# Kernel optimization log

Measured on AMD Instinct MI355X. Metric: run time of the kernel, lower is better.

The kernel has to match this reference:

```python
import jax, jax.numpy as jnp
import numpy as np

NUM_CODES = 4096
EMBED_DIM = 64
BETA = 0.25


def setup_inputs() -> dict:
    key = jax.random.key(0)
    k1, k2 = jax.random.split(key)
    z = jax.random.normal(k1, (8, EMBED_DIM, 64, 64), dtype=jnp.float32)
    weight = jax.random.normal(k2, (NUM_CODES, EMBED_DIM), dtype=jnp.float32)
    return {"z": z, "weight": weight}


def reference(z, weight):
    # z: [B, C, H, W] -> [B, H, W, C]
    z_bhwc = jnp.moveaxis(z, 1, -1)
    z_flat = z_bhwc.reshape(-1, EMBED_DIM)  # [N, d]

    # squared-euclidean distances: ||z||^2 + ||w||^2 - 2 z.w  -> [N, num_codes]
    distance = (
        jnp.sum(z_flat ** 2, axis=1, keepdims=True)
        + jnp.sum(weight ** 2, axis=1)
        - 2.0 * jnp.einsum('bd,nd->bn', z_flat, weight)
    )
    encoding_indices = jnp.argmin(distance, axis=1)  # [N]

    # codebook lookup (gather)
    z_q = weight[encoding_indices].reshape(z_bhwc.shape)  # [B, H, W, C]

    encodings = jax.nn.one_hot(encoding_indices, NUM_CODES, dtype=z.dtype)  # [N, num_codes]
    avg_probs = jnp.mean(encodings, axis=0)
    tiny = 1e-10  # max(1e-10, finfo(fp32).tiny)
    perplexity = jnp.exp(-jnp.sum(avg_probs * jnp.log(avg_probs + tiny)))

    # commitment loss (z_q detached) — eval path, no EMA state update
    loss = BETA * jnp.mean((jax.lax.stop_gradient(z_q) - z_bhwc) ** 2)

    # straight-through estimator
    z_q = z_bhwc + jax.lax.stop_gradient(z_q - z_bhwc)
    z_q = jnp.moveaxis(z_q, -1, 1)  # back to [B, C, H, W]

    return z_q, loss, perplexity, encodings, encoding_indices
```

## Files before the change

### kernel.cpp

```cpp
#include <hip/hip_runtime.h>
#include <math.h>
#include <float.h>

#define ZQ_OFF   0
#define LOSS_OFF 2097152
#define PERP_OFF 2097153
#define ENC_OFF  2097154
#define IDX_OFF  136314882ULL
#define BETA     0.25f


typedef __attribute__((ext_vector_type(8))) short short8;
typedef __attribute__((ext_vector_type(4))) float f32x4;

#define MFMA16(a, b, c) __builtin_amdgcn_mfma_f32_16x16x32_bf16(a, b, c, 0, 0, 0)

__device__ __forceinline__ float bf16_rn(float v, unsigned short* h) {
    unsigned u = __float_as_uint(v);
    unsigned r = (u + 0x7fffu + ((u >> 16) & 1u)) & 0xffff0000u;
    *h = (unsigned short)(r >> 16);
    return __uint_as_float(r);
}
__device__ __forceinline__ void split3(float v, unsigned short* h, unsigned short* m, unsigned short* l) {
    float hf = bf16_rn(v, h);
    float r1 = v - hf;
    float mf = bf16_rn(r1, m);
    float r2 = r1 - mf;
    bf16_rn(r2, l);
}

__global__ void vq_wnorm(const float* __restrict__ w, float* __restrict__ wnorm) {
    int c = blockIdx.x * 256 + threadIdx.x;
    const float4* w4 = (const float4*)(w + ((size_t)c << 6));
    float s = 0.f;
    #pragma unroll
    for (int k = 0; k < 16; ++k) { float4 v = w4[k]; s += v.x*v.x + v.y*v.y + v.z*v.z + v.w*v.w; }
    wnorm[c] = s;
}

__global__ void vq_prep(const float* __restrict__ w, unsigned short* __restrict__ w3) {
    int u = blockIdx.x * 256 + threadIdx.x;
    int c = u >> 5, slot = u & 31;
    if (slot >= 24) return;
    int p = slot >> 3, g = slot & 7;
    float4 v0 = *(const float4*)(w + ((size_t)c << 6) + g * 8);
    float4 v1 = *(const float4*)(w + ((size_t)c << 6) + g * 8 + 4);
    float vv[8] = {v0.x, v0.y, v0.z, v0.w, v1.x, v1.y, v1.z, v1.w};
    short8 o;
    #pragma unroll
    for (int e = 0; e < 8; ++e) {
        unsigned short h, m, l;
        split3(vv[e], &h, &m, &l);
        o[e] = (short)((p == 0) ? h : (p == 1) ? m : l);
    }
    char* dst = (char*)w3 + (size_t)c * 384 + (((unsigned)slot * 16) ^ (((unsigned)c & 7) << 4));
    *(short8*)dst = o;
}

__global__ __launch_bounds__(256, 2) void vq_main(
    const float* __restrict__ z, const float* __restrict__ w,
    const float* __restrict__ wnorm, const unsigned short* __restrict__ w3,
    float* __restrict__ out,
    float* __restrict__ loss_ws, int* __restrict__ ticket, int* __restrict__ hist)
{
    __shared__ __align__(16) char wl[2 * 24576];
    __shared__ float snorm[4096];
    __shared__ int s_widx[64];
    __shared__ int s_flag;

    const int tx   = threadIdx.x;
    const int lane = tx & 63;
    const int wv   = tx >> 6;
    const int lcol = lane & 15;
    const int lkq  = lane >> 4;
    const int base = blockIdx.x * 64;
    const int bb   = base >> 12;
    const int hh   = (base & 4095) >> 6;

    const char* w3b = (const char*)w3;

    {
        const char* s0 = w3b + wv * 6144 + (size_t)lane * 16;
        char* d0 = wl + wv * 6144;
        #pragma unroll
        for (int i = 0; i < 6; ++i)
            __builtin_amdgcn_global_load_lds(
                (const __attribute__((address_space(1))) void*)(s0 + i * 1024),
                (__attribute__((address_space(3))) void*)(d0 + i * 1024), 16, 0, 0);
    }

    float (*zS)[64] = (float (*)[64])(wl + 24576);
    #pragma unroll
    for (int j = 0; j < 4; ++j) {
        int f4 = j * 256 + tx;
        int d  = f4 >> 4, w4i = f4 & 15;
        float4 v = *(const float4*)(z + (((size_t)bb * 64 + d) * 64 + hh) * 64 + w4i * 4);
        *(float4*)&zS[d][w4i * 4] = v;
    }
    #pragma unroll
    for (int j = 0; j < 4; ++j) {
        int c4 = (j * 256 + tx) * 4;
        *(float4*)&snorm[c4] = *(const float4*)(wnorm + c4);
    }
    __syncthreads();

    short8 aH[2], aM[2], aL[2];
    #pragma unroll
    for (int s = 0; s < 2; ++s)
        #pragma unroll
        for (int j = 0; j < 8; ++j) {
            float v = zS[s * 32 + lkq * 8 + j][wv * 16 + lcol];
            unsigned short h, m, l;
            split3(v, &h, &m, &l);
            aH[s][j] = (short)h; aM[s][j] = (short)m; aL[s][j] = (short)l;
        }
    __builtin_amdgcn_sched_barrier(0);
    __builtin_amdgcn_s_barrier();
    __builtin_amdgcn_sched_barrier(0);

    float best[4]; int bidx[4];
    #pragma unroll
    for (int r = 0; r < 4; ++r) { best[r] = FLT_MAX; bidx[r] = 0; }

    float* enc = out + ENC_OFF;
    const unsigned sw = ((unsigned)lcol & 7) << 4;

    #pragma unroll 1
    for (int ch = 0; ch < 64; ++ch) {
        const char* cur = wl + (ch & 1) * 24576;
        char*       nxt = wl + (~ch & 1) * 24576;

        {
            const char* s0 = w3b + (size_t)((ch + 1) & 63) * 24576 + wv * 6144 + (size_t)lane * 16;
            char* d0 = nxt + wv * 6144;
            #pragma unroll
            for (int i = 0; i < 6; ++i)
                __builtin_amdgcn_global_load_lds(
                    (const __attribute__((address_space(1))) void*)(s0 + i * 1024),
                    (__attribute__((address_space(3))) void*)(d0 + i * 1024), 16, 0, 0);
        }
        {
            float2* rowp = (float2*)(enc + ((size_t)(base + ch) << 12));
            #pragma unroll
            for (int j = 0; j < 8; ++j)
                rowp[wv * 512 + j * 64 + lane] = make_float2(0.f, 0.f);
        }
        __builtin_amdgcn_sched_barrier(0);
        asm volatile("s_waitcnt vmcnt(14)" ::: "memory");
        __builtin_amdgcn_s_barrier();
        __builtin_amdgcn_sched_barrier(0);

        {
            const int cbase = ch << 6;
            float wnv[4];
            #pragma unroll
            for (int t = 0; t < 4; ++t) wnv[t] = snorm[cbase + t * 16 + lcol];
            #pragma unroll 2
            for (int t = 0; t < 4; ++t) {
                const int clocal = t * 16 + lcol;
                const char* rowp = cur + clocal * 384;
                short8 bH0 = *(const short8*)(rowp + ((lkq * 16      ) ^ sw));
                short8 bH1 = *(const short8*)(rowp + ((lkq * 16 +  64) ^ sw));
                short8 bM0 = *(const short8*)(rowp + ((lkq * 16 + 128) ^ sw));
                short8 bM1 = *(const short8*)(rowp + ((lkq * 16 + 192) ^ sw));
                short8 bL0 = *(const short8*)(rowp + ((lkq * 16 + 256) ^ sw));
                short8 bL1 = *(const short8*)(rowp + ((lkq * 16 + 320) ^ sw));
                f32x4 c0 = {0.f, 0.f, 0.f, 0.f}, c1 = {0.f, 0.f, 0.f, 0.f}, c2 = {0.f, 0.f, 0.f, 0.f};
                c0 = MFMA16(aH[0], bH0, c0); c0 = MFMA16(aH[1], bH1, c0);
                c1 = MFMA16(aH[0], bM0, c1); c1 = MFMA16(aH[1], bM1, c1);
                c1 = MFMA16(aM[0], bH0, c1); c1 = MFMA16(aM[1], bH1, c1);
                c2 = MFMA16(aM[0], bM0, c2); c2 = MFMA16(aM[1], bM1, c2);
                c2 = MFMA16(aH[0], bL0, c2); c2 = MFMA16(aH[1], bL1, c2);
                c2 = MFMA16(aL[0], bH0, c2); c2 = MFMA16(aL[1], bH1, c2);
                #pragma unroll
                for (int r = 0; r < 4; ++r) {
                    float sdot = (c0[r] + c1[r]) + c2[r];
                    float dd = fmaf(-2.f, sdot, wnv[t]);
                    if (dd < best[r]) { best[r] = dd; bidx[r] = cbase + clocal; }
                }
            }
        }
        __builtin_amdgcn_sched_barrier(0);
        __builtin_amdgcn_s_barrier();
    }

    __syncthreads();

    #pragma unroll
    for (int mm = 1; mm < 16; mm <<= 1) {
        #pragma unroll
        for (int r = 0; r < 4; ++r) {
            float ob = __shfl_xor(best[r], mm, 64);
            int   oi = __shfl_xor(bidx[r], mm, 64);
            if (ob < best[r] || (ob == best[r] && oi < bidx[r])) { best[r] = ob; bidx[r] = oi; }
        }
    }

    if (lcol == 0) {
        const int rowb = wv * 16 + lkq * 4;
        #pragma unroll
        for (int r = 0; r < 4; ++r) {
            int row = rowb + r, bi = bidx[r];
            s_widx[row] = bi;
            out[IDX_OFF + (size_t)(base + row)] = (float)bi;
            atomicAdd(&hist[bi], 1);
            enc[((size_t)(base + row) << 12) + bi] = 1.0f;
        }
    }
    __syncthreads();

    {
        const int row = tx & 63;
        const int dg  = tx >> 6;
        const int wi  = s_widx[row];
        const float* qrow = w + ((size_t)wi << 6);
        float lsum = 0.f;
        #pragma unroll
        for (int dd = 0; dd < 16; ++dd) {
            int d = dg * 16 + dd;
            float qv = qrow[d];
            float zv = z[(((size_t)bb * 64 + d) * 64 + hh) * 64 + row];
            float diff = qv - zv;
            lsum += diff * diff;
            out[ZQ_OFF + (((size_t)bb * 64 + d) * 64 + hh) * 64 + row] = zv + (qv - zv);
        }
        #pragma unroll
        for (int off = 32; off > 0; off >>= 1) lsum += __shfl_down(lsum, off, 64);
        if ((tx & 63) == 0) atomicAdd(loss_ws, lsum);
    }

    __syncthreads();
    if (tx == 0) {
        __threadfence();
        int old = atomicAdd(ticket, 1);
        s_flag = (old == 511) ? 1 : 0;
    }
    __syncthreads();
    if (s_flag) {
        __threadfence();
        float s = 0.f;
        #pragma unroll
        for (int j = 0; j < 16; ++j) {
            int c = tx + j * 256;
            int cnt = atomicAdd(&hist[c], 0);
            float p = (float)cnt * (1.f / 32768.f);
            s += p * logf(p + 1e-10f);
        }
        float* fr = snorm;
        fr[tx] = s;
        __syncthreads();
        for (int off = 128; off > 0; off >>= 1) {
            if (tx < off) fr[tx] += fr[tx + off];
            __syncthreads();
        }
        if (tx == 0) {
            out[LOSS_OFF] = BETA * atomicAdd(loss_ws, 0.f) / 2097152.f;
            out[PERP_OFF] = expf(-fr[0]);
        }
    }
}

extern "C" void kernel_launch(void* const* d_in, const int* in_sizes, int n_in,
                              void* d_out, int out_size, void* d_ws, size_t ws_size,
                              hipStream_t stream)
{
    const float* z = (const float*)d_in[0];
    const float* w = (const float*)d_in[1];
    float* out     = (float*)d_out;
    float* loss_ws = (float*)d_ws;
    int*   ticket  = (int*)((char*)d_ws + 4);
    int*   hist    = (int*)((char*)d_ws + 16);
    float* wnorm   = (float*)((char*)d_ws + 16400);
    unsigned short* w3 = (unsigned short*)((char*)d_ws + 32800);
    (void)ws_size; (void)in_sizes; (void)n_in; (void)out_size;

    hipMemsetAsync(d_ws, 0, 16 + 4096 * sizeof(int), stream);
    vq_wnorm<<<16, 256, 0, stream>>>(w, wnorm);
    vq_prep<<<512, 256, 0, stream>>>(w, w3);
    vq_main<<<512, 256, 0, stream>>>(z, w, wnorm, w3, out, loss_ws, ticket, hist);
}
```

Measured before the change: 612.9 us.

## Split waves 2x2 over rows and codes, add nontemporal stores

Each wave now handles 32 rows and 32 codes per chunk instead of 16 rows and 64 codes. This halves the LDS B-fragment loads per MFMA, because each B fragment is reused across two A tiles. A cross-wave reduction through shared memory merges the two code halves. The zeroing of the one-hot encodings, the index writes and the z_q writes use nontemporal stores, and the zero-store slot order is rotated. The change raises register use for the doubled A fragments and best/index state, which may put the 2-wave-per-SIMD launch bound under pressure.

```diff
diff --git a/kernel.cpp b/kernel.cpp
--- a/kernel.cpp
+++ b/kernel.cpp
@@ -12,6 +12,7 @@
 
 typedef __attribute__((ext_vector_type(8))) short short8;
 typedef __attribute__((ext_vector_type(4))) float f32x4;
+typedef __attribute__((ext_vector_type(2))) float f32x2;
 
 #define MFMA16(a, b, c) __builtin_amdgcn_mfma_f32_16x16x32_bf16(a, b, c, 0, 0, 0)
 
@@ -68,14 +69,16 @@
     __shared__ int s_widx[64];
     __shared__ int s_flag;
 
-    const int tx   = threadIdx.x;
-    const int lane = tx & 63;
-    const int wv   = tx >> 6;
-    const int lcol = lane & 15;
-    const int lkq  = lane >> 4;
-    const int base = blockIdx.x * 64;
-    const int bb   = base >> 12;
-    const int hh   = (base & 4095) >> 6;
+    const int tx    = threadIdx.x;
+    const int lane  = tx & 63;
+    const int wv    = tx >> 6;
+    const int rh    = wv & 1;
+    const int chalf = wv >> 1;
+    const int lcol  = lane & 15;
+    const int lkq   = lane >> 4;
+    const int base  = blockIdx.x * 64;
+    const int bb    = base >> 12;
+    const int hh    = (base & 4095) >> 6;
 
     const char* w3b = (const char*)w3;
 
@@ -104,26 +107,31 @@
     }
     __syncthreads();
 
-    short8 aH[2], aM[2], aL[2];
-    #pragma unroll
-    for (int s = 0; s < 2; ++s)
-        #pragma unroll
-        for (int j = 0; j < 8; ++j) {
-            float v = zS[s * 32 + lkq * 8 + j][wv * 16 + lcol];
-            unsigned short h, m, l;
-            split3(v, &h, &m, &l);
-            aH[s][j] = (short)h; aM[s][j] = (short)m; aL[s][j] = (short)l;
-        }
+    short8 aH[2][2], aM[2][2], aL[2][2];
+    #pragma unroll
+    for (int u = 0; u < 2; ++u)
+        #pragma unroll
+        for (int s = 0; s < 2; ++s)
+            #pragma unroll
+            for (int j = 0; j < 8; ++j) {
+                float v = zS[s * 32 + lkq * 8 + j][rh * 32 + u * 16 + lcol];
+                unsigned short h, m, l;
+                split3(v, &h, &m, &l);
+                aH[u][s][j] = (short)h; aM[u][s][j] = (short)m; aL[u][s][j] = (short)l;
+            }
     __builtin_amdgcn_sched_barrier(0);
     __builtin_amdgcn_s_barrier();
     __builtin_amdgcn_sched_barrier(0);
 
-    float best[4]; int bidx[4];
-    #pragma unroll
-    for (int r = 0; r < 4; ++r) { best[r] = FLT_MAX; bidx[r] = 0; }
+    float best[2][4]; int bidx[2][4];
+    #pragma unroll
+    for (int u = 0; u < 2; ++u)
+        #pragma unroll
+        for (int r = 0; r < 4; ++r) { best[u][r] = FLT_MAX; bidx[u][r] = 0; }
 
     float* enc = out + ENC_OFF;
     const unsigned sw = ((unsigned)lcol & 7) << 4;
+    const f32x2 zero2 = {0.f, 0.f};
 
     #pragma unroll 1
     for (int ch = 0; ch < 64; ++ch) {
@@ -140,10 +148,12 @@
                     (__attribute__((address_space(3))) void*)(d0 + i * 1024), 16, 0, 0);
         }
         {
-            float2* rowp = (float2*)(enc + ((size_t)(base + ch) << 12));
-            #pragma unroll
-            for (int j = 0; j < 8; ++j)
-                rowp[wv * 512 + j * 64 + lane] = make_float2(0.f, 0.f);
+            f32x2* rowp = (f32x2*)(enc + ((size_t)(base + ch) << 12));
+            #pragma unroll
+            for (int j = 0; j < 8; ++j) {
+                int slot = (wv * 512 + j * 64 + lane + 7) & 2047;
+                __builtin_nontemporal_store(zero2, rowp + slot);
+            }
         }
         __builtin_amdgcn_sched_barrier(0);
         asm volatile("s_waitcnt vmcnt(14)" ::: "memory");
@@ -152,12 +162,9 @@
 
         {
             const int cbase = ch << 6;
-            float wnv[4];
-            #pragma unroll
-            for (int t = 0; t < 4; ++t) wnv[t] = snorm[cbase + t * 16 + lcol];
-            #pragma unroll 2
-            for (int t = 0; t < 4; ++t) {
-                const int clocal = t * 16 + lcol;
+            #pragma unroll
+            for (int t = 0; t < 2; ++t) {
+                const int clocal = chalf * 32 + t * 16 + lcol;
                 const char* rowp = cur + clocal * 384;
                 short8 bH0 = *(const short8*)(rowp + ((lkq * 16      ) ^ sw));
                 short8 bH1 = *(const short8*)(rowp + ((lkq * 16 +  64) ^ sw));
@@ -165,18 +172,22 @@
                 short8 bM1 = *(const short8*)(rowp + ((lkq * 16 + 192) ^ sw));
                 short8 bL0 = *(const short8*)(rowp + ((lkq * 16 + 256) ^ sw));
                 short8 bL1 = *(const short8*)(rowp + ((lkq * 16 + 320) ^ sw));
-                f32x4 c0 = {0.f, 0.f, 0.f, 0.f}, c1 = {0.f, 0.f, 0.f, 0.f}, c2 = {0.f, 0.f, 0.f, 0.f};
-                c0 = MFMA16(aH[0], bH0, c0); c0 = MFMA16(aH[1], bH1, c0);
-                c1 = MFMA16(aH[0], bM0, c1); c1 = MFMA16(aH[1], bM1, c1);
-                c1 = MFMA16(aM[0], bH0, c1); c1 = MFMA16(aM[1], bH1, c1);
-                c2 = MFMA16(aM[0], bM0, c2); c2 = MFMA16(aM[1], bM1, c2);
-                c2 = MFMA16(aH[0], bL0, c2); c2 = MFMA16(aH[1], bL1, c2);
-                c2 = MFMA16(aL[0], bH0, c2); c2 = MFMA16(aL[1], bH1, c2);
+                const float wnv = snorm[cbase + clocal];
                 #pragma unroll
-                for (int r = 0; r < 4; ++r) {
-                    float sdot = (c0[r] + c1[r]) + c2[r];
-                    float dd = fmaf(-2.f, sdot, wnv[t]);
-                    if (dd < best[r]) { best[r] = dd; bidx[r] = cbase + clocal; }
+                for (int u = 0; u < 2; ++u) {
+                    f32x4 c0 = {0.f,0.f,0.f,0.f}, c1 = {0.f,0.f,0.f,0.f}, c2 = {0.f,0.f,0.f,0.f};
+                    c0 = MFMA16(aH[u][0], bH0, c0); c0 = MFMA16(aH[u][1], bH1, c0);
+                    c1 = MFMA16(aH[u][0], bM0, c1); c1 = MFMA16(aH[u][1], bM1, c1);
+                    c1 = MFMA16(aM[u][0], bH0, c1); c1 = MFMA16(aM[u][1], bH1, c1);
+                    c2 = MFMA16(aM[u][0], bM0, c2); c2 = MFMA16(aM[u][1], bM1, c2);
+                    c2 = MFMA16(aH[u][0], bL0, c2); c2 = MFMA16(aH[u][1], bL1, c2);
+                    c2 = MFMA16(aL[u][0], bH0, c2); c2 = MFMA16(aL[u][1], bH1, c2);
+                    #pragma unroll
+                    for (int r = 0; r < 4; ++r) {
+                        float sdot = (c0[r] + c1[r]) + c2[r];
+                        float dd = fmaf(-2.f, sdot, wnv);
+                        if (dd < best[u][r]) { best[u][r] = dd; bidx[u][r] = cbase + clocal; }
+                    }
                 }
             }
         }
@@ -187,25 +198,41 @@
     __syncthreads();
 
     #pragma unroll
-    for (int mm = 1; mm < 16; mm <<= 1) {
-        #pragma unroll
-        for (int r = 0; r < 4; ++r) {
-            float ob = __shfl_xor(best[r], mm, 64);
-            int   oi = __shfl_xor(bidx[r], mm, 64);
-            if (ob < best[r] || (ob == best[r] && oi < bidx[r])) { best[r] = ob; bidx[r] = oi; }
-        }
-    }
-
+    for (int u = 0; u < 2; ++u)
+        #pragma unroll
+        for (int mm = 1; mm < 16; mm <<= 1)
+            #pragma unroll
+            for (int r = 0; r < 4; ++r) {
+                float ob = __shfl_xor(best[u][r], mm, 64);
+                int   oi = __shfl_xor(bidx[u][r], mm, 64);
+                if (ob < best[u][r] || (ob == best[u][r] && oi < bidx[u][r])) {
+                    best[u][r] = ob; bidx[u][r] = oi;
+                }
+            }
+
+    float2* s_red = (float2*)snorm;
     if (lcol == 0) {
-        const int rowb = wv * 16 + lkq * 4;
-        #pragma unroll
-        for (int r = 0; r < 4; ++r) {
-            int row = rowb + r, bi = bidx[r];
-            s_widx[row] = bi;
-            out[IDX_OFF + (size_t)(base + row)] = (float)bi;
-            atomicAdd(&hist[bi], 1);
-            enc[((size_t)(base + row) << 12) + bi] = 1.0f;
-        }
+        #pragma unroll
+        for (int u = 0; u < 2; ++u)
+            #pragma unroll
+            for (int r = 0; r < 4; ++r) {
+                int row = rh * 32 + u * 16 + lkq * 4 + r;
+                s_red[row * 2 + chalf] = make_float2(best[u][r], __int_as_float(bidx[u][r]));
+            }
+    }
+    __syncthreads();
+
+    if (tx < 64) {
+        float2 a = s_red[tx * 2], b2 = s_red[tx * 2 + 1];
+        int ai = __float_as_int(a.y), bi2 = __float_as_int(b2.y);
+        int bi; float bv;
+        if (a.x < b2.x || (a.x == b2.x && ai < bi2)) { bv = a.x; bi = ai; }
+        else                                          { bv = b2.x; bi = bi2; }
+        (void)bv;
+        s_widx[tx] = bi;
+        __builtin_nontemporal_store((float)bi, out + IDX_OFF + (size_t)(base + tx));
+        atomicAdd(&hist[bi], 1);
+        __builtin_nontemporal_store(1.0f, enc + ((size_t)(base + tx) << 12) + bi);
     }
     __syncthreads();
 
@@ -222,7 +249,8 @@
             float zv = z[(((size_t)bb * 64 + d) * 64 + hh) * 64 + row];
             float diff = qv - zv;
             lsum += diff * diff;
-            out[ZQ_OFF + (((size_t)bb * 64 + d) * 64 + hh) * 64 + row] = zv + (qv - zv);
+            __builtin_nontemporal_store(zv + (qv - zv),
+                out + ZQ_OFF + (((size_t)bb * 64 + d) * 64 + hh) * 64 + row);
         }
         #pragma unroll
         for (int off = 32; off > 0; off >>= 1) lsum += __shfl_down(lsum, off, 64);
```

After: 601.0 us, median of 2. No clear change (-1.9%).
